# Performance work log

Measured on AMD Instinct MI355X. Metric: run time of the kernel, lower is better.

Reference implementation:

```python
import math
import jax, jax.numpy as jnp
import numpy as np

N_HEADS = 16


def setup_inputs() -> dict:
    key = jax.random.key(0)
    k1, k2 = jax.random.split(key)
    N, H, C, T = 2, N_HEADS, 64, 2048
    qkv = jax.random.normal(k1, (N, H * 3 * C, T), dtype=jnp.float32)
    mask = jax.random.randint(k2, (N, 1, T), 0, 2).astype(bool) | (jnp.arange(T)[None, None, :] < T // 2)
    return {"qkv": qkv, "mask": mask}


def reference(qkv, mask):
    bs, width, length = qkv.shape
    ch = width // (3 * N_HEADS)
    qkv_r = qkv.reshape(bs * N_HEADS, 3 * ch, length)
    q, k, v = qkv_r[:, :ch], qkv_r[:, ch:2 * ch], qkv_r[:, 2 * ch:]
    scale = 1.0 / math.sqrt(math.sqrt(ch))
    # [bH, T, T] scores in float32 (matches weight.float())
    weight = jnp.einsum('bct,bcs->bts', q * scale, k * scale).astype(jnp.float32)
    inv = ~mask[:, 0, :]                                   # [N, T] True = pad
    m = inv[:, None, :] | inv[:, :, None]                  # [N, T, T]
    m = jnp.broadcast_to(m[:, None], (bs, N_HEADS, length, length)).reshape(-1, length, length)
    weight = jnp.where(m, jnp.finfo(weight.dtype).min, weight)
    weight = jax.nn.softmax(weight, axis=-1)
    a = jnp.einsum('bts,bcs->bct', weight, v)              # [bH, C, T]
    return a.reshape(bs, -1, length)
```

## Files before the change

kernel.cpp:

```cpp
#include <hip/hip_runtime.h>
#include <hip/hip_bf16.h>
#include <stdint.h>

namespace {

constexpr int T_LEN = 2048;
constexpr int NROWS = 192;
constexpr int QBLK  = 64;
constexpr int NBH   = 32;
constexpr int KT_STRIDE = 72;
constexpr int TILE_ELEMS = 64 * KT_STRIDE;

typedef float f32x4 __attribute__((ext_vector_type(4)));
typedef short bf16x8 __attribute__((ext_vector_type(8)));
typedef short bf16x4 __attribute__((ext_vector_type(4)));

__device__ __forceinline__ unsigned short f2bf(float f) {
  union { float f; unsigned u; } v; v.f = f;
  unsigned r = v.u + 0x7fffu + ((v.u >> 16) & 1u);
  return (unsigned short)(r >> 16);
}
__device__ __forceinline__ unsigned pack2(float a, float b) {
  return (unsigned)f2bf(a) | ((unsigned)f2bf(b) << 16);
}
__device__ __forceinline__ float fast_exp2(float x) {
#if __has_builtin(__builtin_amdgcn_exp2f)
  return __builtin_amdgcn_exp2f(x);
#else
  return exp2f(x);
#endif
}
__device__ __forceinline__ f32x4 mfma_16x16x16_bf16(bf16x4 a, bf16x4 b, f32x4 c) {
#if __has_builtin(__builtin_amdgcn_mfma_f32_16x16x16bf16_1k)
  return __builtin_amdgcn_mfma_f32_16x16x16bf16_1k(a, b, c, 0, 0, 0);
#else
  asm("v_mfma_f32_16x16x16_bf16 %0, %1, %2, %0" : "+v"(c) : "v"(a), "v"(b));
  return c;
#endif
}

}

__global__ void nm_kernel(const unsigned char* __restrict__ raw,
                          unsigned char* __restrict__ outm, int n) {
  int stride = (raw[1] != 0) ? 1 : ((raw[4] != 0) ? 4 : 8);
  int i = blockIdx.x * blockDim.x + threadIdx.x;
  if (i < n) outm[i] = (raw[(size_t)i * stride] != 0) ? 1 : 0;
}


__global__ __launch_bounds__(256) void tq3_kernel(const float* __restrict__ qkv,
                                                  short* __restrict__ qtg,
                                                  short* __restrict__ ktg) {
  __shared__ float tile[64][65];
  const int t = threadIdx.x;
  const int which = blockIdx.z;
  const int bh = blockIdx.y;
  const int bx = blockIdx.x;
  const int s0 = bx * 64;
  const float* src = qkv + (size_t)bh * NROWS * T_LEN + (size_t)which * 64 * T_LEN;
  const int c = t >> 2;
  #pragma unroll
  for (int p = 0; p < 4; ++p) {
    int col = (t & 3) * 4 + p * 16;
    float4 v = *(const float4*)&src[(size_t)c * T_LEN + s0 + col];
    tile[c][col] = v.x; tile[c][col + 1] = v.y;
    tile[c][col + 2] = v.z; tile[c][col + 3] = v.w;
  }
  __syncthreads();
  const float scale = which ? 1.0f : 0.18033688011112042f;
  const int s = t & 63;
  #pragma unroll
  for (int p = 0; p < 2; ++p) {
    int jc = (t >> 6) * 2 + p;
    bf16x4 o0, o1;
    #pragma unroll
    for (int i = 0; i < 4; ++i) {
      o0[i] = (short)f2bf(tile[jc * 8 + i][s] * scale);
      o1[i] = (short)f2bf(tile[jc * 8 + 4 + i][s] * scale);
    }
    short* d = which
      ? (ktg + (size_t)(bh * 32 + bx) * TILE_ELEMS + s * KT_STRIDE + jc * 8)
      : (qtg + (size_t)bh * T_LEN * 64 + (size_t)(s0 + s) * 64 + jc * 8);
    *(bf16x4*)d = o0;
    *(bf16x4*)(d + 4) = o1;
  }
}

__global__ __launch_bounds__(256) void cv3_kernel(const float* __restrict__ qkv,
                                                  short* __restrict__ vtg) {
  int cid = blockIdx.x * 256 + threadIdx.x;
  int bh = cid >> 14;
  int rem = cid & 16383;
  int c = rem >> 8;
  int cg = rem & 255;
  int grp = cg >> 3, jin = cg & 7;
  const float* src = qkv + (size_t)bh * NROWS * T_LEN + (size_t)(128 + c) * T_LEN + cg * 8;
  float4 a = *(const float4*)src;
  float4 b = *(const float4*)(src + 4);
  bf16x4 o0, o1;
  o0[0] = (short)f2bf(a.x); o0[1] = (short)f2bf(a.y);
  o0[2] = (short)f2bf(a.z); o0[3] = (short)f2bf(a.w);
  o1[0] = (short)f2bf(b.x); o1[1] = (short)f2bf(b.y);
  o1[2] = (short)f2bf(b.z); o1[3] = (short)f2bf(b.w);
  short* d = vtg + (size_t)(bh * 32 + grp) * TILE_ELEMS + c * KT_STRIDE + jin * 8;
  *(bf16x4*)d = o0;
  *(bf16x4*)(d + 4) = o1;
}


__global__ __launch_bounds__(512) void attn6_kernel(const short* __restrict__ qtg,
                                                    const short* __restrict__ ktg,
                                                    const short* __restrict__ vtg,
                                                    const unsigned char* __restrict__ maskn,
                                                    float* __restrict__ out) {
  __shared__ __align__(16) short Kt[2][TILE_ELEMS];
  __shared__ __align__(16) short Vs[2][TILE_ELEMS];
  __shared__ __align__(16) unsigned char Ms[T_LEN];

  const int tid  = threadIdx.x;
  const int lane = tid & 63;
  const int wv   = tid >> 6;
  const int tw   = wv & 3;
  const int sh   = wv >> 2;
  const int l15  = lane & 15;
  const int g    = lane >> 4;

  int id = blockIdx.x;
  id = (id & 7) * 128 + (id >> 3);
  const int bh = id >> 5;
  const int t0 = (id & 31) * QBLK;
  const int nb = bh >> 4;

  if (tid < 256) ((uint2*)Ms)[tid] = ((const uint2*)(maskn + (size_t)nb * T_LEN))[tid];

  const int t_lane = t0 + tw * 16 + l15;
  const short* Qrow = qtg + (size_t)bh * T_LEN * 64 + (size_t)t_lane * 64;
  const bf16x8 qf0 = *(const bf16x8*)(Qrow + g * 8);
  const bf16x8 qf1 = *(const bf16x8*)(Qrow + 32 + g * 8);

  const bf16x8* __restrict__ kbase = (const bf16x8*)(ktg + (size_t)bh * 32 * TILE_ELEMS);
  const bf16x8* __restrict__ vbase = (const bf16x8*)(vtg + (size_t)bh * 32 * TILE_ELEMS);

  {
    const bf16x8* ks = kbase;
    const bf16x8* vs = vbase;
    ((bf16x8*)Kt[0])[tid] = ks[tid];
    ((bf16x8*)Vs[0])[tid] = vs[tid];
    if (tid < 64) {
      ((bf16x8*)Kt[0])[tid + 512] = ks[tid + 512];
      ((bf16x8*)Vs[0])[tid + 512] = vs[tid + 512];
    }
  }
  __syncthreads();
  const bool invt = (Ms[t_lane] == 0);

  f32x4 acc[4];
  #pragma unroll
  for (int i = 0; i < 4; ++i) acc[i] = (f32x4){0.f, 0.f, 0.f, 0.f};
  float l_part = 0.0f;

  int cur = 0;
  for (int sb = 0; sb < T_LEN / 64; ++sb) {
    bf16x8 k0, k1, v0, v1;
    const bool more = (sb + 1 < T_LEN / 64);
    if (more) {
      const bf16x8* ks = kbase + (size_t)(sb + 1) * (TILE_ELEMS / 8);
      const bf16x8* vs = vbase + (size_t)(sb + 1) * (TILE_ELEMS / 8);
      k0 = ks[tid]; v0 = vs[tid];
      if (tid < 64) { k1 = ks[tid + 512]; v1 = vs[tid + 512]; }
    }

    const short* Ktc = Kt[cur];
    const short* Vsc = Vs[cur];
    const int s0 = sb * 64;
    #pragma unroll
    for (int sti = 0; sti < 2; ++sti) {
      const int st = sh * 2 + sti;
      const int srow = st * 16 + l15;
      bf16x8 kf0 = *(const bf16x8*)&Ktc[srow * KT_STRIDE + g * 8];
      bf16x8 kf1 = *(const bf16x8*)&Ktc[srow * KT_STRIDE + 32 + g * 8];
      f32x4 S = (f32x4){0.f, 0.f, 0.f, 0.f};
      S = __builtin_amdgcn_mfma_f32_16x16x32_bf16(kf0, qf0, S, 0, 0, 0);
      S = __builtin_amdgcn_mfma_f32_16x16x32_bf16(kf1, qf1, S, 0, 0, 0);

      const unsigned m4 = *(const unsigned*)&Ms[s0 + st * 16 + g * 4];
      float p0, p1, p2, p3;
      {
        float x0 = ((m4 & 0x000000ffu) ? S[0] : -1.0e30f);
        float x1 = ((m4 & 0x0000ff00u) ? S[1] : -1.0e30f);
        float x2 = ((m4 & 0x00ff0000u) ? S[2] : -1.0e30f);
        float x3 = ((m4 & 0xff000000u) ? S[3] : -1.0e30f);
        p0 = fast_exp2(invt ? 0.0f : x0);
        p1 = fast_exp2(invt ? 0.0f : x1);
        p2 = fast_exp2(invt ? 0.0f : x2);
        p3 = fast_exp2(invt ? 0.0f : x3);
      }
      l_part += (p0 + p1) + (p2 + p3);

      union { bf16x4 v; __hip_bfloat162 h[2]; } pf;
      pf.h[0] = __float22bfloat162_rn(float2{p0, p1});
      pf.h[1] = __float22bfloat162_rn(float2{p2, p3});

      #pragma unroll
      for (int cb = 0; cb < 4; ++cb) {
        bf16x4 vf = *(const bf16x4*)&Vsc[(cb * 16 + l15) * KT_STRIDE + st * 16 + g * 4];
        acc[cb] = mfma_16x16x16_bf16(vf, pf.v, acc[cb]);
      }
    }

    if (more) {
      short* Ktn = Kt[cur ^ 1];
      short* Vsn = Vs[cur ^ 1];
      ((bf16x8*)Ktn)[tid] = k0;
      ((bf16x8*)Vsn)[tid] = v0;
      if (tid < 64) {
        ((bf16x8*)Ktn)[tid + 512] = k1;
        ((bf16x8*)Vsn)[tid + 512] = v1;
      }
    }
    __syncthreads();
    cur ^= 1;
  }

  float* scratch = (float*)Kt;
  const int trow = tw * 16 + l15;
  if (wv >= 4) {
    float* row = scratch + trow * 68;
    #pragma unroll
    for (int cb = 0; cb < 4; ++cb) *(f32x4*)&row[cb * 16 + g * 4] = acc[cb];
    row[64 + g] = l_part;
  }
  __syncthreads();
  if (wv < 4) {
    const float* row = scratch + trow * 68;
    #pragma unroll
    for (int cb = 0; cb < 4; ++cb) acc[cb] += *(const f32x4*)&row[cb * 16 + g * 4];
    l_part += row[64 + g];

    l_part += __shfl_xor(l_part, 16, 64);
    l_part += __shfl_xor(l_part, 32, 64);
    const float il = 1.0f / l_part;
    const size_t out_base = (size_t)bh * 64 * T_LEN;
    #pragma unroll
    for (int cb = 0; cb < 4; ++cb) {
      #pragma unroll
      for (int r = 0; r < 4; ++r) {
        int c = cb * 16 + g * 4 + r;
        out[out_base + (size_t)c * T_LEN + t_lane] = acc[cb][r] * il;
      }
    }
  }
}


__global__ __launch_bounds__(256) void attn_fb_kernel(const float* __restrict__ qkv,
                                                      const unsigned char* __restrict__ maskn,
                                                      float* __restrict__ out) {
  __shared__ __align__(16) short Kt[QBLK * KT_STRIDE];
  __shared__ __align__(16) short Vs[64 * KT_STRIDE];
  __shared__ __align__(16) unsigned char Ms[T_LEN];

  const int tid  = threadIdx.x;
  const int lane = tid & 63;
  const int wv   = tid >> 6;
  const int l15  = lane & 15;
  const int g    = lane >> 4;

  const int bh = blockIdx.y;
  const int nb = bh >> 4;
  const int t0 = blockIdx.x * QBLK;

  const float* __restrict__ Qg = qkv + (size_t)bh * NROWS * T_LEN;
  const float* __restrict__ Kg = Qg + (size_t)64 * T_LEN;
  const float* __restrict__ Vg = Qg + (size_t)128 * T_LEN;

  {
    const uint2* src = (const uint2*)(maskn + (size_t)nb * T_LEN);
    ((uint2*)Ms)[tid] = src[tid];
  }
  {
    const int c2 = (tid >> 6) * 2;
    const int s  = tid & 63;
    #pragma unroll
    for (int p = 0; p < 8; ++p) {
      int c = p * 8 + c2;
      float f0 = Qg[(size_t)c * T_LEN + t0 + s] * 0.125f;
      float f1 = Qg[(size_t)(c + 1) * T_LEN + t0 + s] * 0.125f;
      *(unsigned*)&Kt[s * KT_STRIDE + c] = pack2(f0, f1);
    }
  }
  __syncthreads();

  bf16x8 qf0 = *(const bf16x8*)&Kt[(wv * 16 + l15) * KT_STRIDE + g * 8];
  bf16x8 qf1 = *(const bf16x8*)&Kt[(wv * 16 + l15) * KT_STRIDE + 32 + g * 8];
  const int t_lane = t0 + wv * 16 + l15;
  const bool invt = (Ms[t_lane] == 0);

  f32x4 acc[4];
  #pragma unroll
  for (int i = 0; i < 4; ++i) acc[i] = (f32x4){0.f, 0.f, 0.f, 0.f};
  float m_run = -3.0e38f;
  float l_run = 0.0f;

  for (int sb = 0; sb < T_LEN / 64; ++sb) {
    const int s0 = sb * 64;
    __syncthreads();
    {
      const int c2 = (tid >> 6) * 2;
      const int s  = tid & 63;
      #pragma unroll
      for (int p = 0; p < 8; ++p) {
        int c = p * 8 + c2;
        float f0 = Kg[(size_t)c * T_LEN + s0 + s];
        float f1 = Kg[(size_t)(c + 1) * T_LEN + s0 + s];
        *(unsigned*)&Kt[s * KT_STRIDE + c] = pack2(f0, f1);
      }
    }
    {
      const int cv = (tid >> 5);
      const int s2 = tid & 31;
      #pragma unroll
      for (int p = 0; p < 8; ++p) {
        int c = p * 8 + cv;
        float2 f = *(const float2*)&Vg[(size_t)c * T_LEN + s0 + 2 * s2];
        *(unsigned*)&Vs[c * KT_STRIDE + 2 * s2] = pack2(f.x, f.y);
      }
    }
    __syncthreads();

    #pragma unroll
    for (int st = 0; st < 4; ++st) {
      const int srow = st * 16 + l15;
      bf16x8 kf0 = *(const bf16x8*)&Kt[srow * KT_STRIDE + g * 8];
      bf16x8 kf1 = *(const bf16x8*)&Kt[srow * KT_STRIDE + 32 + g * 8];
      f32x4 S = (f32x4){0.f, 0.f, 0.f, 0.f};
      S = __builtin_amdgcn_mfma_f32_16x16x32_bf16(kf0, qf0, S, 0, 0, 0);
      S = __builtin_amdgcn_mfma_f32_16x16x32_bf16(kf1, qf1, S, 0, 0, 0);

      const unsigned m4 = *(const unsigned*)&Ms[s0 + st * 16 + g * 4];
      float vals[4];
      #pragma unroll
      for (int r = 0; r < 4; ++r) {
        float x = ((m4 >> (8 * r)) & 0xffu) ? S[r] : -1.0e30f;
        vals[r] = invt ? 0.0f : x;
      }
      float pm = fmaxf(fmaxf(vals[0], vals[1]), fmaxf(vals[2], vals[3]));
      pm = fmaxf(pm, __shfl_xor(pm, 16, 64));
      pm = fmaxf(pm, __shfl_xor(pm, 32, 64));
      const float newm = fmaxf(m_run, pm);
      const float alpha = fast_exp2((m_run - newm) * 1.44269504f);
      float p0 = fast_exp2((vals[0] - newm) * 1.44269504f);
      float p1 = fast_exp2((vals[1] - newm) * 1.44269504f);
      float p2 = fast_exp2((vals[2] - newm) * 1.44269504f);
      float p3 = fast_exp2((vals[3] - newm) * 1.44269504f);
      float ps = (p0 + p1) + (p2 + p3);
      ps += __shfl_xor(ps, 16, 64);
      ps += __shfl_xor(ps, 32, 64);
      l_run = l_run * alpha + ps;
      m_run = newm;
      if (__any(alpha < 1.0f)) {
        #pragma unroll
        for (int cb = 0; cb < 4; ++cb)
          #pragma unroll
          for (int r = 0; r < 4; ++r) acc[cb][r] *= alpha;
      }
      bf16x4 pf;
      pf[0] = (short)f2bf(p0); pf[1] = (short)f2bf(p1);
      pf[2] = (short)f2bf(p2); pf[3] = (short)f2bf(p3);
      #pragma unroll
      for (int cb = 0; cb < 4; ++cb) {
        bf16x4 vf = *(const bf16x4*)&Vs[(cb * 16 + l15) * KT_STRIDE + st * 16 + g * 4];
        acc[cb] = mfma_16x16x16_bf16(vf, pf, acc[cb]);
      }
    }
  }

  const float il = 1.0f / l_run;
  const size_t out_base = (size_t)bh * 64 * T_LEN;
  #pragma unroll
  for (int cb = 0; cb < 4; ++cb) {
    #pragma unroll
    for (int r = 0; r < 4; ++r) {
      int c = cb * 16 + g * 4 + r;
      out[out_base + (size_t)c * T_LEN + t_lane] = acc[cb][r] * il;
    }
  }
}


extern "C" void kernel_launch(void* const* d_in, const int* in_sizes, int n_in,
                              void* d_out, int out_size, void* d_ws, size_t ws_size,
                              hipStream_t stream) {
  (void)n_in; (void)out_size;
  const float* qkv = (const float*)d_in[0];
  const unsigned char* mraw = (const unsigned char*)d_in[1];
  float* out = (float*)d_out;
  const int mask_elems = in_sizes[1];

  const size_t QSZ = (size_t)NBH * T_LEN * 64 * sizeof(short);
  const size_t TSZ = (size_t)NBH * 32 * TILE_ELEMS * sizeof(short);
  const size_t need = QSZ + 2 * TSZ + (size_t)mask_elems;
  if (ws_size >= need) {
    short* qtg = (short*)d_ws;
    short* ktg = (short*)((char*)d_ws + QSZ);
    short* vtg = (short*)((char*)d_ws + QSZ + TSZ);
    unsigned char* maskn = (unsigned char*)d_ws + QSZ + 2 * TSZ;
    nm_kernel<<<(mask_elems + 255) / 256, 256, 0, stream>>>(mraw, maskn, mask_elems);
    tq3_kernel<<<dim3(T_LEN / 64, NBH, 2), 256, 0, stream>>>(qkv, qtg, ktg);
    cv3_kernel<<<(NBH * 64 * 256) / 256, 256, 0, stream>>>(qkv, vtg);
    attn6_kernel<<<dim3(NBH * 32), 512, 0, stream>>>(qtg, ktg, vtg, maskn, out);
  } else {
    unsigned char* maskn = (unsigned char*)d_ws;
    nm_kernel<<<(mask_elems + 255) / 256, 256, 0, stream>>>(mraw, maskn, mask_elems);
    attn_fb_kernel<<<dim3(T_LEN / QBLK, NBH), 256, 0, stream>>>(qkv, maskn, out);
  }
}
```

Baseline: 91.56 us.

## Use direct global-to-LDS loads and additive float mask bias in attention

The K/V tile prefetch now uses global_load_lds, so tiles go straight from global memory into the alternate shared buffer without staging in registers. The byte mask in LDS and its per-element selects are replaced by a float additive bias row read from global memory. Padded query rows are handled by zeroing their Q scale and pointing them at a zero bias row. This cuts VGPR pressure and ALU work in the inner loop, but adds global bias reads and relies on the async LDS-load semantics being correct with the existing barrier.

```diff
diff --git a/kernel.cpp b/kernel.cpp
--- a/kernel.cpp
+++ b/kernel.cpp
@@ -10,6 +10,7 @@
 constexpr int NBH   = 32;
 constexpr int KT_STRIDE = 72;
 constexpr int TILE_ELEMS = 64 * KT_STRIDE;
+constexpr int TILE_BYTES = TILE_ELEMS * 2;
 
 typedef float f32x4 __attribute__((ext_vector_type(4)));
 typedef short bf16x8 __attribute__((ext_vector_type(8)));
@@ -38,6 +39,11 @@
   return c;
 #endif
 }
+__device__ __forceinline__ void gload_lds16(const void* g, void* l) {
+  __builtin_amdgcn_global_load_lds(
+      (const __attribute__((address_space(1))) unsigned int*)g,
+      (__attribute__((address_space(3))) unsigned int*)l, 16, 0, 0);
+}
 
 }
 
@@ -48,8 +54,17 @@
   if (i < n) outm[i] = (raw[(size_t)i * stride] != 0) ? 1 : 0;
 }
 
-
-__global__ __launch_bounds__(256) void tq3_kernel(const float* __restrict__ qkv,
+__global__ void bias9_kernel(const unsigned char* __restrict__ raw,
+                             float* __restrict__ bias, int n) {
+  int stride = (raw[1] != 0) ? 1 : ((raw[4] != 0) ? 4 : 8);
+  int i = blockIdx.x * blockDim.x + threadIdx.x;
+  if (i < n) bias[i] = (raw[(size_t)i * stride] != 0) ? 0.0f : -1.0e30f;
+  else if (i < n + T_LEN) bias[i] = 0.0f;
+}
+
+
+__global__ __launch_bounds__(256) void tq9_kernel(const float* __restrict__ qkv,
+                                                  const unsigned char* __restrict__ mraw,
                                                   short* __restrict__ qtg,
                                                   short* __restrict__ ktg) {
   __shared__ float tile[64][65];
@@ -68,8 +83,16 @@
     tile[c][col + 2] = v.z; tile[c][col + 3] = v.w;
   }
   __syncthreads();
-  const float scale = which ? 1.0f : 0.18033688011112042f;
   const int s = t & 63;
+  float scale;
+  if (which) {
+    scale = 1.0f;
+  } else {
+    const int mstride = (mraw[1] != 0) ? 1 : ((mraw[4] != 0) ? 4 : 8);
+    const int nb = bh >> 4;
+    const bool live = mraw[((size_t)nb * T_LEN + s0 + s) * mstride] != 0;
+    scale = live ? 0.18033688011112042f : 0.0f;
+  }
   #pragma unroll
   for (int p = 0; p < 2; ++p) {
     int jc = (t >> 6) * 2 + p;
@@ -109,14 +132,14 @@
 }
 
 
-__global__ __launch_bounds__(512) void attn6_kernel(const short* __restrict__ qtg,
+__global__ __launch_bounds__(512) void attn9_kernel(const short* __restrict__ qtg,
                                                     const short* __restrict__ ktg,
                                                     const short* __restrict__ vtg,
-                                                    const unsigned char* __restrict__ maskn,
+                                                    const float* __restrict__ bias,
+                                                    int mask_elems,
                                                     float* __restrict__ out) {
   __shared__ __align__(16) short Kt[2][TILE_ELEMS];
   __shared__ __align__(16) short Vs[2][TILE_ELEMS];
-  __shared__ __align__(16) unsigned char Ms[T_LEN];
 
   const int tid  = threadIdx.x;
   const int lane = tid & 63;
@@ -132,28 +155,23 @@
   const int t0 = (id & 31) * QBLK;
   const int nb = bh >> 4;
 
-  if (tid < 256) ((uint2*)Ms)[tid] = ((const uint2*)(maskn + (size_t)nb * T_LEN))[tid];
-
   const int t_lane = t0 + tw * 16 + l15;
   const short* Qrow = qtg + (size_t)bh * T_LEN * 64 + (size_t)t_lane * 64;
   const bf16x8 qf0 = *(const bf16x8*)(Qrow + g * 8);
   const bf16x8 qf1 = *(const bf16x8*)(Qrow + 32 + g * 8);
 
-  const bf16x8* __restrict__ kbase = (const bf16x8*)(ktg + (size_t)bh * 32 * TILE_ELEMS);
-  const bf16x8* __restrict__ vbase = (const bf16x8*)(vtg + (size_t)bh * 32 * TILE_ELEMS);
-
-  {
-    const bf16x8* ks = kbase;
-    const bf16x8* vs = vbase;
-    ((bf16x8*)Kt[0])[tid] = ks[tid];
-    ((bf16x8*)Vs[0])[tid] = vs[tid];
-    if (tid < 64) {
-      ((bf16x8*)Kt[0])[tid + 512] = ks[tid + 512];
-      ((bf16x8*)Vs[0])[tid + 512] = vs[tid + 512];
-    }
-  }
+  const float bt = bias[(size_t)nb * T_LEN + t_lane];
+  const float* __restrict__ brow = bias + ((bt != 0.0f) ? (size_t)mask_elems
+                                                        : (size_t)nb * T_LEN);
+
+  const char* __restrict__ kt0 = (const char*)(ktg + (size_t)bh * 32 * TILE_ELEMS);
+  const char* __restrict__ vt0 = (const char*)(vtg + (size_t)bh * 32 * TILE_ELEMS);
+
+  gload_lds16(kt0 + wv * 1024 + lane * 16, (char*)Kt[0] + wv * 1024);
+  gload_lds16(vt0 + wv * 1024 + lane * 16, (char*)Vs[0] + wv * 1024);
+  if (wv == 0) gload_lds16(kt0 + 8192 + lane * 16, (char*)Kt[0] + 8192);
+  if (wv == 1) gload_lds16(vt0 + 8192 + lane * 16, (char*)Vs[0] + 8192);
   __syncthreads();
-  const bool invt = (Ms[t_lane] == 0);
 
   f32x4 acc[4];
   #pragma unroll
@@ -162,13 +180,15 @@
 
   int cur = 0;
   for (int sb = 0; sb < T_LEN / 64; ++sb) {
-    bf16x8 k0, k1, v0, v1;
-    const bool more = (sb + 1 < T_LEN / 64);
-    if (more) {
-      const bf16x8* ks = kbase + (size_t)(sb + 1) * (TILE_ELEMS / 8);
-      const bf16x8* vs = vbase + (size_t)(sb + 1) * (TILE_ELEMS / 8);
-      k0 = ks[tid]; v0 = vs[tid];
-      if (tid < 64) { k1 = ks[tid + 512]; v1 = vs[tid + 512]; }
+    if (sb + 1 < T_LEN / 64) {
+      const char* ks = kt0 + (size_t)(sb + 1) * TILE_BYTES;
+      const char* vs = vt0 + (size_t)(sb + 1) * TILE_BYTES;
+      char* Ktn = (char*)Kt[cur ^ 1];
+      char* Vsn = (char*)Vs[cur ^ 1];
+      gload_lds16(ks + wv * 1024 + lane * 16, Ktn + wv * 1024);
+      gload_lds16(vs + wv * 1024 + lane * 16, Vsn + wv * 1024);
+      if (wv == 0) gload_lds16(ks + 8192 + lane * 16, Ktn + 8192);
+      if (wv == 1) gload_lds16(vs + 8192 + lane * 16, Vsn + 8192);
     }
 
     const short* Ktc = Kt[cur];
@@ -184,18 +204,11 @@
       S = __builtin_amdgcn_mfma_f32_16x16x32_bf16(kf0, qf0, S, 0, 0, 0);
       S = __builtin_amdgcn_mfma_f32_16x16x32_bf16(kf1, qf1, S, 0, 0, 0);
 
-      const unsigned m4 = *(const unsigned*)&Ms[s0 + st * 16 + g * 4];
-      float p0, p1, p2, p3;
-      {
-        float x0 = ((m4 & 0x000000ffu) ? S[0] : -1.0e30f);
-        float x1 = ((m4 & 0x0000ff00u) ? S[1] : -1.0e30f);
-        float x2 = ((m4 & 0x00ff0000u) ? S[2] : -1.0e30f);
-        float x3 = ((m4 & 0xff000000u) ? S[3] : -1.0e30f);
-        p0 = fast_exp2(invt ? 0.0f : x0);
-        p1 = fast_exp2(invt ? 0.0f : x1);
-        p2 = fast_exp2(invt ? 0.0f : x2);
-        p3 = fast_exp2(invt ? 0.0f : x3);
-      }
+      const f32x4 b4 = *(const f32x4*)&brow[s0 + st * 16 + g * 4];
+      float p0 = fast_exp2(S[0] + b4[0]);
+      float p1 = fast_exp2(S[1] + b4[1]);
+      float p2 = fast_exp2(S[2] + b4[2]);
+      float p3 = fast_exp2(S[3] + b4[3]);
       l_part += (p0 + p1) + (p2 + p3);
 
       union { bf16x4 v; __hip_bfloat162 h[2]; } pf;
@@ -209,16 +222,6 @@
       }
     }
 
-    if (more) {
-      short* Ktn = Kt[cur ^ 1];
-      short* Vsn = Vs[cur ^ 1];
-      ((bf16x8*)Ktn)[tid] = k0;
-      ((bf16x8*)Vsn)[tid] = v0;
-      if (tid < 64) {
-        ((bf16x8*)Ktn)[tid + 512] = k1;
-        ((bf16x8*)Vsn)[tid + 512] = v1;
-      }
-    }
     __syncthreads();
     cur ^= 1;
   }
@@ -400,16 +403,17 @@
 
   const size_t QSZ = (size_t)NBH * T_LEN * 64 * sizeof(short);
   const size_t TSZ = (size_t)NBH * 32 * TILE_ELEMS * sizeof(short);
-  const size_t need = QSZ + 2 * TSZ + (size_t)mask_elems;
+  const size_t BSZ = (size_t)(mask_elems + T_LEN) * sizeof(float);
+  const size_t need = QSZ + 2 * TSZ + BSZ;
   if (ws_size >= need) {
     short* qtg = (short*)d_ws;
     short* ktg = (short*)((char*)d_ws + QSZ);
     short* vtg = (short*)((char*)d_ws + QSZ + TSZ);
-    unsigned char* maskn = (unsigned char*)d_ws + QSZ + 2 * TSZ;
-    nm_kernel<<<(mask_elems + 255) / 256, 256, 0, stream>>>(mraw, maskn, mask_elems);
-    tq3_kernel<<<dim3(T_LEN / 64, NBH, 2), 256, 0, stream>>>(qkv, qtg, ktg);
+    float* bias = (float*)((char*)d_ws + QSZ + 2 * TSZ);
+    bias9_kernel<<<(mask_elems + T_LEN + 255) / 256, 256, 0, stream>>>(mraw, bias, mask_elems);
+    tq9_kernel<<<dim3(T_LEN / 64, NBH, 2), 256, 0, stream>>>(qkv, mraw, qtg, ktg);
     cv3_kernel<<<(NBH * 64 * 256) / 256, 256, 0, stream>>>(qkv, vtg);
-    attn6_kernel<<<dim3(NBH * 32), 512, 0, stream>>>(qtg, ktg, vtg, maskn, out);
+    attn9_kernel<<<dim3(NBH * 32), 512, 0, stream>>>(qtg, ktg, vtg, bias, mask_elems, out);
   } else {
     unsigned char* maskn = (unsigned char*)d_ws;
     nm_kernel<<<(mask_elems + 255) / 256, 256, 0, stream>>>(mraw, maskn, mask_elems);
```

Result: no change. 91.37 us (-0.2%).
